# Performance work log

Hardware: AMD Instinct MI355X
Metric: run time of the kernel (lower is better)

Reference implementation:

```python
import jax, jax.numpy as jnp
import numpy as np

E = 1024      # embed_dim
H = 16        # num_heads
HD = E // H   # head_dim = 64


def setup_inputs() -> dict:
    key = jax.random.key(0)
    ks = jax.random.split(key, 8)
    T, B, S = 1024, 4, 1024
    return {
        "query": jax.random.normal(ks[0], (T, B, E), jnp.float32),
        "key": jax.random.normal(ks[1], (S, B, E), jnp.float32),
        "value": jax.random.normal(ks[2], (S, B, E), jnp.float32),
        "attn_mask": jax.random.normal(ks[3], (T, S), jnp.float32),
        "key_padding_mask": jax.random.randint(ks[4], (B, S), 0, 2, jnp.int32),
        "in_proj_weight": jax.random.normal(ks[5], (3 * E, E), jnp.float32) * 0.02,
        "in_proj_bias": jnp.zeros((3 * E,), jnp.float32),
        "out_w": jax.random.normal(ks[6], (E, E), jnp.float32) * 0.02,
        "out_b": jnp.zeros((E,), jnp.float32),
    }


def reference(query, key, value, attn_mask, key_padding_mask,
              in_proj_weight, in_proj_bias, out_w, out_b):
    T, B, _ = query.shape
    S = key.shape[0]
    w_q, w_k, w_v = jnp.split(in_proj_weight, 3, axis=0)   # each [E, E]
    b_q, b_k, b_v = jnp.split(in_proj_bias, 3, axis=0)
    q = query @ w_q.T + b_q                                # [T, B, E]
    k = key @ w_k.T + b_k                                  # [S, B, E]
    v = value @ w_v.T + b_v                                # [S, B, E]
    # [len, B, E] -> [B*H, len, HD]
    q = q.reshape(T, B * H, HD).transpose(1, 0, 2) / jnp.sqrt(jnp.float32(HD))
    k = k.reshape(S, B * H, HD).transpose(1, 0, 2)
    v = v.reshape(S, B * H, HD).transpose(1, 0, 2)
    scores = jnp.einsum('bth,bsh->bts', q, k)              # [B*H, T, S]
    scores = scores + attn_mask[None]                      # float additive mask
    pad = key_padding_mask.astype(bool)                    # [B, S]
    pad = jnp.broadcast_to(pad[:, None, None, :], (B, H, 1, S)).reshape(B * H, 1, S)
    scores = jnp.where(pad, -jnp.inf, scores)
    weights = jax.nn.softmax(scores, axis=-1)              # dropout p=0 -> identity
    out = jnp.einsum('bts,bsh->bth', weights, v)           # [B*H, T, HD]
    out = out.transpose(1, 0, 2).reshape(T, B, E)
    out = out @ out_w.T + out_b
    weights_avg = weights.reshape(B, H, T, S).mean(axis=1) # sum/H == mean
    return out, weights_avg
```

## Files before the change

### kernel.cpp

```cpp
#include <hip/hip_runtime.h>
#include <stdint.h>

typedef short bf16x8 __attribute__((ext_vector_type(8)));
typedef float f32x4  __attribute__((ext_vector_type(4)));

#define LOG2E_F 1.4426950408889634f
#define QSCALE_F 0.1803368801111204f

__device__ __forceinline__ unsigned short f2bf(float f) {
    unsigned int u = __float_as_uint(f);
    return (unsigned short)((u + 0x7FFFu + ((u >> 16) & 1u)) >> 16);
}

__device__ __forceinline__ unsigned short f2bfu(float f) {
    return (unsigned short)((__float_as_uint(f) + 0x8000u) >> 16);
}

__device__ __forceinline__ uint4 pack8(float4 a, float4 b) {
    union { unsigned short us[8]; uint4 v; } p;
    p.us[0] = f2bf(a.x); p.us[1] = f2bf(a.y); p.us[2] = f2bf(a.z); p.us[3] = f2bf(a.w);
    p.us[4] = f2bf(b.x); p.us[5] = f2bf(b.y); p.us[6] = f2bf(b.z); p.us[7] = f2bf(b.w);
    return p.v;
}

__device__ __forceinline__ void gload_lds16(const unsigned short* g, unsigned short* l) {
    __builtin_amdgcn_global_load_lds(
        (const __attribute__((address_space(1))) void*)g,
        (__attribute__((address_space(3))) void*)l, 16, 0, 0);
}

__device__ __forceinline__ int tauinv(int x) {
    const int j4 = x & 7, hh = x & 32, bb = x & 24;
    if (j4 < 4) return hh + ((bb & 15) >> 2) * 8 + (bb >> 4) * 4 + j4;
    const int b2 = bb + 4;
    return hh + ((b2 & 15) >> 2) * 8 + (b2 >> 4) * 4 + (j4 - 4);
}

__global__ __launch_bounds__(256)
void cvt_kernel(const float* __restrict__ q, const float* __restrict__ k,
                const float* __restrict__ v, const float* __restrict__ w,
                const float* __restrict__ ow,
                uint4* __restrict__ Xb, uint4* __restrict__ Wb, uint4* __restrict__ OWb)
{
    const unsigned g = blockIdx.x * 256 + threadIdx.x;
    const float* src;
    uint4* dst;
    if (g < 1572864u) {
        dst = Xb + g;
        if (g < 524288u)        src = q + (size_t)g * 8;
        else if (g < 1048576u)  src = k + (size_t)(g - 524288u) * 8;
        else                    src = v + (size_t)(g - 1048576u) * 8;
    } else if (g < 1966080u) {
        src = w + (size_t)(g - 1572864u) * 8;
        dst = Wb + (g - 1572864u);
    } else {
        src = ow + (size_t)(g - 1966080u) * 8;
        dst = OWb + (g - 1966080u);
    }
    float4 a = *(const float4*)src;
    float4 b = *(const float4*)(src + 4);
    *dst = pack8(a, b);
}

__global__ __launch_bounds__(256)
void mtr_kernel(const float* __restrict__ m, float* __restrict__ mt)
{
    __shared__ float tile[64][65];
    const int bt = (blockIdx.x & 15) << 6;
    const int bs = (blockIdx.x >> 4) << 6;
    const int tx = threadIdx.x & 63;
    const int ty = threadIdx.x >> 6;
#pragma unroll
    for (int i = 0; i < 64; i += 4)
        tile[ty + i][tx] = m[(size_t)(bt + ty + i) * 1024 + bs + tx];
    __syncthreads();
#pragma unroll
    for (int i = 0; i < 64; i += 4) {
        const int s = bs + ty + i;
        mt[(size_t)(s >> 2) * 4096 + (bt + tx) * 4 + (s & 3)] = tile[tx][ty + i];
    }
}

__global__ __launch_bounds__(256)
void qkv_proj_kernel(const unsigned short* __restrict__ Xb, const unsigned short* __restrict__ Wb,
                     const float* __restrict__ bias,
                     unsigned short* __restrict__ Qb, unsigned short* __restrict__ Kb,
                     unsigned short* __restrict__ Vtb)
{
    const int z = blockIdx.z;
    const int j   = blockIdx.x;
    const int xcd = j & 7, idx = j >> 3;
    const int row0 = ((xcd << 2) + (idx >> 3)) * 128;
    const int col0 = (idx & 7) * 128;
    const int wofs = z << 10;

    const unsigned short* A = Xb + (size_t)z * 4194304;
    const unsigned short* B = Wb;

    __shared__ __align__(16) unsigned short As[128 * 32];
    __shared__ __align__(16) unsigned short Bs[128 * 32];

    const int tid  = threadIdx.x;
    const int lane = tid & 63;
    const int wv   = tid >> 6;
    const int wr   = wv >> 1, wc = wv & 1;
    const int c16  = lane & 15;
    const int kof  = (lane >> 4) << 3;

    const f32x4 zero4 = {0.f, 0.f, 0.f, 0.f};
    f32x4 acc[4][4];
#pragma unroll
    for (int m = 0; m < 4; ++m)
#pragma unroll
        for (int n = 0; n < 4; ++n) acc[m][n] = zero4;

    const unsigned short* gA = A + (size_t)(row0 + wv * 16 + (lane >> 2)) * 1024 + ((lane & 3) << 3);
    const unsigned short* gB = B + (size_t)(wofs + col0 + wv * 16 + (lane >> 2)) * 1024 + ((lane & 3) << 3);
    unsigned short* lA = As + tid * 8;
    unsigned short* lB = Bs + tid * 8;

    const int arow = wr * 64 + c16;
    const int brow = wc * 64 + c16;

    for (int k0 = 0; k0 < 1024; k0 += 32) {
        __syncthreads();
        gload_lds16(gA + k0,         lA);
        gload_lds16(gA + k0 + 65536, lA + 2048);
        gload_lds16(gB + k0,         lB);
        gload_lds16(gB + k0 + 65536, lB + 2048);
        __syncthreads();

        bf16x8 af[4], bfr[4];
#pragma unroll
        for (int m = 0; m < 4; ++m)
            af[m] = *(const bf16x8*)&As[(arow + m * 16) * 32 + kof];
#pragma unroll
        for (int n = 0; n < 4; ++n)
            bfr[n] = *(const bf16x8*)&Bs[(brow + n * 16) * 32 + kof];
#pragma unroll
        for (int m = 0; m < 4; ++m)
#pragma unroll
            for (int n = 0; n < 4; ++n)
                acc[m][n] = __builtin_amdgcn_mfma_f32_16x16x32_bf16(af[m], bfr[n], acc[m][n], 0, 0, 0);
    }

    const int ccol = c16;
    const int crow = (lane >> 4) << 2;
#pragma unroll
    for (int n = 0; n < 4; ++n) {
        const int gc   = col0 + wc * 64 + n * 16 + ccol;
        const float bv = bias[wofs + gc];
        const int head = gc >> 6, d = gc & 63;
#pragma unroll
        for (int m = 0; m < 4; ++m) {
            const int tt = (row0 + wr * 64 + m * 16 + crow) >> 2;
            if (z == 2) {
                const int R     = tt >> 7;
                const int tileb = (tt >> 6) & 1;
                const int col   = tauinv(tt & 63);
                const int lc    = tileb * 8 + (col >> 3);
                const int jj    = col & 7;
                const int pc    = lc ^ (d & 7);
                const size_t of = ((size_t)(d) << 7) + (pc << 3) + jj;
#pragma unroll
                for (int r = 0; r < 4; ++r) {
                    const int bh = (r << 4) + head;
                    Vtb[(((size_t)bh * 8 + R) << 13) + of] = f2bf(acc[m][n][r] + bv);
                }
            } else {
#pragma unroll
                for (int r = 0; r < 4; ++r) {
                    const int bh = (r << 4) + head;
                    const float vv = acc[m][n][r] + bv;
                    if (z == 0) Qb[((size_t)bh << 16) + ((size_t)tt << 6) + d] = f2bf(vv * QSCALE_F);
                    else        Kb[((size_t)bh << 16) + ((size_t)tt << 6) + d] = f2bf(vv);
                }
            }
        }
    }
}

__global__ __launch_bounds__(512)
void flash_kernel(const unsigned short* __restrict__ Qb, const unsigned short* __restrict__ Kb,
                  const unsigned short* __restrict__ Vtb, const float* __restrict__ maskT,
                  const int* __restrict__ padmask,
                  float* __restrict__ rl_buf, unsigned short* __restrict__ attn_out)
{
    const int j   = blockIdx.x;
    const int xcd = j & 7, idx = j >> 3;
    const int bh  = xcd * 8 + (idx >> 3);
    const int t0  = (idx & 7) << 7;
    const int b   = bh >> 4, h = bh & 15;

    __shared__ __align__(16) unsigned short Ks[2][2][64 * 64];
    __shared__ __align__(16) unsigned short Vs[2][64 * 128];

    const int tid  = threadIdx.x;
    const int lane = tid & 63;
    const int wv   = tid >> 6;
    const int kof  = (lane >> 4) << 3;
    const int gq   = lane >> 4;
    const int c16  = lane & 15;
    const int g4   = gq << 2;

    const unsigned short* Qbase = Qb  + ((size_t)bh << 16);
    const unsigned short* Kbase = Kb  + ((size_t)bh << 16);
    const unsigned short* Vsig  = Vtb + ((size_t)bh << 16);

    bf16x8 qf[2];
#pragma unroll
    for (int kk = 0; kk < 2; ++kk)
        qf[kk] = *(const bf16x8*)(Qbase + ((size_t)(t0 + wv * 16 + c16) << 6) + kk * 32 + kof);

    const bf16x8 ones = {16256, 16256, 16256, 16256, 16256, 16256, 16256, 16256};

    const f32x4 zero4 = {0.f, 0.f, 0.f, 0.f};
    f32x4 acco[4];
#pragma unroll
    for (int nd = 0; nd < 4; ++nd) acco[nd] = zero4;
    f32x4 acc_l = zero4;

    const int strow = tid >> 3;
    const unsigned short* gK = Kbase + ((size_t)strow << 6) + (((tid & 7) ^ (strow & 7)) << 3);
    unsigned short* lK0a = &Ks[0][0][tid * 8];
    unsigned short* lK0b = &Ks[0][1][tid * 8];
    unsigned short* lK1a = &Ks[1][0][tid * 8];
    unsigned short* lK1b = &Ks[1][1][tid * 8];
    unsigned short* lV0  = &Vs[0][tid * 8];
    unsigned short* lV1  = &Vs[1][tid * 8];

    const int tr2 = t0 + wv * 16 + c16;

    gload_lds16(gK,        lK0a);
    gload_lds16(gK + 4096, lK0b);
    gload_lds16(Vsig + tid * 8,        lV0);
    gload_lds16(Vsig + 4096 + tid * 8, lV0 + 4096);
    __syncthreads();

    for (int rd = 0; rd < 8; ++rd) {
        const int cur = rd & 1;
        const int s0  = rd << 7;

        if (rd < 7) {
            const size_t kofs = (size_t)(s0 + 128) << 6;
            gload_lds16(gK + kofs,        cur ? lK0a : lK1a);
            gload_lds16(gK + kofs + 4096, cur ? lK0b : lK1b);
            const size_t vofs = (size_t)(rd + 1) << 13;
            gload_lds16(Vsig + vofs + tid * 8,        cur ? lV0 : lV1);
            gload_lds16(Vsig + vofs + 4096 + tid * 8, (cur ? lV0 : lV1) + 4096);
        }

        f32x4 accsA[4], accsB[4];
#pragma unroll
        for (int n = 0; n < 4; ++n) { accsA[n] = zero4; accsB[n] = zero4; }
        __builtin_amdgcn_s_setprio(1);
#pragma unroll
        for (int n = 0; n < 4; ++n) {
            const int rowK = n * 16 + c16;
            const int swzK = rowK & 7;
            const int o0 = rowK * 64 + ((gq ^ swzK) << 3);
            const int o1 = rowK * 64 + (((4 + gq) ^ swzK) << 3);
            bf16x8 kfA0 = *(const bf16x8*)&Ks[cur][0][o0];
            bf16x8 kfA1 = *(const bf16x8*)&Ks[cur][0][o1];
            accsA[n] = __builtin_amdgcn_mfma_f32_16x16x32_bf16(kfA0, qf[0], accsA[n], 0, 0, 0);
            accsA[n] = __builtin_amdgcn_mfma_f32_16x16x32_bf16(kfA1, qf[1], accsA[n], 0, 0, 0);
            bf16x8 kfB0 = *(const bf16x8*)&Ks[cur][1][o0];
            bf16x8 kfB1 = *(const bf16x8*)&Ks[cur][1][o1];
            accsB[n] = __builtin_amdgcn_mfma_f32_16x16x32_bf16(kfB0, qf[0], accsB[n], 0, 0, 0);
            accsB[n] = __builtin_amdgcn_mfma_f32_16x16x32_bf16(kfB1, qf[1], accsB[n], 0, 0, 0);
        }
        __builtin_amdgcn_s_setprio(0);

#pragma unroll
        for (int tile = 0; tile < 2; ++tile) {
            const int s0t = s0 + tile * 64;
            f32x4* accs = tile ? accsB : accsA;

            float4 mk[4];
            int4 pd[4];
#pragma unroll
            for (int n = 0; n < 4; ++n) {
                const int srow = s0t + n * 16 + g4;
                pd[n] = *(const int4*)(padmask + (b << 10) + srow);
                mk[n] = *(const float4*)(maskT + (size_t)(srow >> 2) * 4096 + tr2 * 4);
            }

            union { unsigned short us[16]; bf16x8 v[2]; } pk;
#pragma unroll
            for (int n = 0; n < 4; ++n) {
                float x0 = fmaf(mk[n].x, LOG2E_F, accs[n][0]);
                float x1 = fmaf(mk[n].y, LOG2E_F, accs[n][1]);
                float x2 = fmaf(mk[n].z, LOG2E_F, accs[n][2]);
                float x3 = fmaf(mk[n].w, LOG2E_F, accs[n][3]);
                if (pd[n].x) x0 = -1e30f;
                if (pd[n].y) x1 = -1e30f;
                if (pd[n].z) x2 = -1e30f;
                if (pd[n].w) x3 = -1e30f;
                pk.us[n * 4 + 0] = f2bfu(__builtin_amdgcn_exp2f(x0));
                pk.us[n * 4 + 1] = f2bfu(__builtin_amdgcn_exp2f(x1));
                pk.us[n * 4 + 2] = f2bfu(__builtin_amdgcn_exp2f(x2));
                pk.us[n * 4 + 3] = f2bfu(__builtin_amdgcn_exp2f(x3));
            }

            __builtin_amdgcn_s_setprio(1);
#pragma unroll
            for (int hhh = 0; hhh < 2; ++hhh) {
                bf16x8 pf = pk.v[hhh];
                const int lc = tile * 8 + hhh * 4 + gq;
#pragma unroll
                for (int nd = 0; nd < 4; ++nd) {
                    const int rowV = nd * 16 + c16;
                    bf16x8 vf = *(const bf16x8*)&Vs[cur][rowV * 128 + ((lc ^ (rowV & 7)) << 3)];
                    acco[nd] = __builtin_amdgcn_mfma_f32_16x16x32_bf16(pf, vf, acco[nd], 0, 0, 0);
                }
                acc_l = __builtin_amdgcn_mfma_f32_16x16x32_bf16(pf, ones, acc_l, 0, 0, 0);
            }
            __builtin_amdgcn_s_setprio(0);
        }

        if (rd < 7) __syncthreads();
    }

#pragma unroll
    for (int r = 0; r < 4; ++r) {
        const int t = t0 + wv * 16 + g4 + r;
        const float rl = 1.0f / acc_l[r];
        if (c16 == 0)
            rl_buf[(bh << 10) + t] = rl;
#pragma unroll
        for (int nd = 0; nd < 4; ++nd) {
            const int d = nd * 16 + c16;
            attn_out[((size_t)t * 4 + b) * 1024 + h * 64 + d] = f2bf(acco[nd][r] * rl);
        }
    }
}

__global__ __launch_bounds__(256)
void wavg_kernel(const unsigned short* __restrict__ Qb, const unsigned short* __restrict__ Kb,
                 const float* __restrict__ attn_mask, const int* __restrict__ padmask,
                 const float* __restrict__ rl_buf, float* __restrict__ wout)
{
    const int j   = blockIdx.x;
    const int xcd = j & 7;
    const int b   = xcd >> 1;
    const int rr  = ((j >> 3) << 1) + (xcd & 1);
    const int t0  = (rr >> 4) << 6;
    const int s0  = (rr & 15) << 6;

    __shared__ __align__(16) unsigned short Qs[2][64 * 72];
    __shared__ __align__(16) unsigned short Ks2[2][64 * 72];

    const int tid  = threadIdx.x;
    const int lane = tid & 63;
    const int wv   = tid >> 6;
    const int wr   = wv >> 1, wc = wv & 1;
    const int kof  = (lane >> 4) << 3;
    const int srow_st = tid >> 2;
    const int scol_st = (tid & 3) << 4;

    const int t_base = t0 + wr * 32 + ((lane >> 4) << 2);
    const int s_base = s0 + wc * 32 + (lane & 15);

    int pad2[2];
#pragma unroll
    for (int nn = 0; nn < 2; ++nn) pad2[nn] = padmask[(b << 10) + s_base + nn * 16];

    float maskv[2][2][4];
#pragma unroll
    for (int mm = 0; mm < 2; ++mm)
#pragma unroll
        for (int r = 0; r < 4; ++r)
#pragma unroll
            for (int nn = 0; nn < 2; ++nn)
                maskv[mm][nn][r] = attn_mask[(size_t)(t_base + mm * 16 + r) * 1024 + s_base + nn * 16] * LOG2E_F;

    float wsum[2][2][4];
#pragma unroll
    for (int mm = 0; mm < 2; ++mm)
#pragma unroll
        for (int nn = 0; nn < 2; ++nn)
#pragma unroll
            for (int r = 0; r < 4; ++r) wsum[mm][nn][r] = 0.f;

    const unsigned short* qsrc = Qb + ((size_t)(t0 + srow_st) << 6) + scol_st;
    const unsigned short* ksrc = Kb + ((size_t)(s0 + srow_st) << 6) + scol_st;
    const size_t bh0 = (size_t)(b << 4) << 16;

    uint4 q0 = *(const uint4*)(qsrc + bh0);
    uint4 q1 = *(const uint4*)(qsrc + bh0 + 8);
    uint4 k0 = *(const uint4*)(ksrc + bh0);
    uint4 k1 = *(const uint4*)(ksrc + bh0 + 8);
    *(uint4*)&Qs[0][srow_st * 72 + scol_st]      = q0;
    *(uint4*)&Qs[0][srow_st * 72 + scol_st + 8]  = q1;
    *(uint4*)&Ks2[0][srow_st * 72 + scol_st]     = k0;
    *(uint4*)&Ks2[0][srow_st * 72 + scol_st + 8] = k1;
    q0 = *(const uint4*)(qsrc + bh0 + 65536);
    q1 = *(const uint4*)(qsrc + bh0 + 65536 + 8);
    k0 = *(const uint4*)(ksrc + bh0 + 65536);
    k1 = *(const uint4*)(ksrc + bh0 + 65536 + 8);
    __syncthreads();

#pragma unroll 2
    for (int h = 0; h < 16; ++h) {
        const int cur = h & 1;
        const int bh  = (b << 4) + h;

        if (h < 15) {
            *(uint4*)&Qs[cur ^ 1][srow_st * 72 + scol_st]      = q0;
            *(uint4*)&Qs[cur ^ 1][srow_st * 72 + scol_st + 8]  = q1;
            *(uint4*)&Ks2[cur ^ 1][srow_st * 72 + scol_st]     = k0;
            *(uint4*)&Ks2[cur ^ 1][srow_st * 72 + scol_st + 8] = k1;
        }
        if (h < 14) {
            const size_t of = bh0 + (size_t)(h + 2) * 65536;
            q0 = *(const uint4*)(qsrc + of);
            q1 = *(const uint4*)(qsrc + of + 8);
            k0 = *(const uint4*)(ksrc + of);
            k1 = *(const uint4*)(ksrc + of + 8);
        }

        float rlv[2][4];
#pragma unroll
        for (int mm = 0; mm < 2; ++mm)
#pragma unroll
            for (int r = 0; r < 4; ++r)
                rlv[mm][r] = rl_buf[(bh << 10) + t_base + mm * 16 + r];

        const f32x4 zero4 = {0.f, 0.f, 0.f, 0.f};
        f32x4 accs[2][2];
#pragma unroll
        for (int mm = 0; mm < 2; ++mm)
#pragma unroll
            for (int nn = 0; nn < 2; ++nn) accs[mm][nn] = zero4;
#pragma unroll
        for (int nn = 0; nn < 2; ++nn) {
            bf16x8 kf0 = *(const bf16x8*)&Ks2[cur][(wc * 32 + nn * 16 + (lane & 15)) * 72 + kof];
            bf16x8 kf1 = *(const bf16x8*)&Ks2[cur][(wc * 32 + nn * 16 + (lane & 15)) * 72 + 32 + kof];
#pragma unroll
            for (int mm = 0; mm < 2; ++mm) {
                bf16x8 qf0 = *(const bf16x8*)&Qs[cur][(wr * 32 + mm * 16 + (lane & 15)) * 72 + kof];
                bf16x8 qf1 = *(const bf16x8*)&Qs[cur][(wr * 32 + mm * 16 + (lane & 15)) * 72 + 32 + kof];
                accs[mm][nn] = __builtin_amdgcn_mfma_f32_16x16x32_bf16(qf0, kf0, accs[mm][nn], 0, 0, 0);
                accs[mm][nn] = __builtin_amdgcn_mfma_f32_16x16x32_bf16(qf1, kf1, accs[mm][nn], 0, 0, 0);
            }
        }
#pragma unroll
        for (int mm = 0; mm < 2; ++mm)
#pragma unroll
            for (int nn = 0; nn < 2; ++nn)
#pragma unroll
                for (int r = 0; r < 4; ++r)
                    if (!pad2[nn]) {
                        float x = accs[mm][nn][r] + maskv[mm][nn][r];
                        wsum[mm][nn][r] += __builtin_amdgcn_exp2f(x) * rlv[mm][r];
                    }

        if (h < 15) __syncthreads();
    }

#pragma unroll
    for (int mm = 0; mm < 2; ++mm)
#pragma unroll
        for (int nn = 0; nn < 2; ++nn)
#pragma unroll
            for (int r = 0; r < 4; ++r)
                wout[((size_t)b << 20) + (size_t)(t_base + mm * 16 + r) * 1024 + s_base + nn * 16]
                    = wsum[mm][nn][r] * 0.0625f;
}

__global__ __launch_bounds__(256)
void out_proj_kernel(const unsigned short* __restrict__ A, const unsigned short* __restrict__ Wb,
                     const float* __restrict__ bias, float* __restrict__ out)
{
    const int j   = blockIdx.x;
    const int xcd = j & 7, idx = j >> 3;
    const int row0 = ((xcd << 2) + (idx >> 3)) * 128;
    const int col0 = (idx & 7) * 128;

    __shared__ __align__(16) unsigned short As[128 * 32];
    __shared__ __align__(16) unsigned short Bs[128 * 32];

    const int tid  = threadIdx.x;
    const int lane = tid & 63;
    const int wv   = tid >> 6;
    const int wr   = wv >> 1, wc = wv & 1;
    const int c16  = lane & 15;
    const int kof  = (lane >> 4) << 3;

    const f32x4 zero4 = {0.f, 0.f, 0.f, 0.f};
    f32x4 acc[4][4];
#pragma unroll
    for (int m = 0; m < 4; ++m)
#pragma unroll
        for (int n = 0; n < 4; ++n) acc[m][n] = zero4;

    const unsigned short* gA = A  + (size_t)(row0 + wv * 16 + (lane >> 2)) * 1024 + ((lane & 3) << 3);
    const unsigned short* gB = Wb + (size_t)(col0 + wv * 16 + (lane >> 2)) * 1024 + ((lane & 3) << 3);
    unsigned short* lA = As + tid * 8;
    unsigned short* lB = Bs + tid * 8;

    const int arow = wr * 64 + c16;
    const int brow = wc * 64 + c16;

    for (int k0 = 0; k0 < 1024; k0 += 32) {
        __syncthreads();
        gload_lds16(gA + k0,         lA);
        gload_lds16(gA + k0 + 65536, lA + 2048);
        gload_lds16(gB + k0,         lB);
        gload_lds16(gB + k0 + 65536, lB + 2048);
        __syncthreads();

        bf16x8 af[4], bfr[4];
#pragma unroll
        for (int m = 0; m < 4; ++m)
            af[m] = *(const bf16x8*)&As[(arow + m * 16) * 32 + kof];
#pragma unroll
        for (int n = 0; n < 4; ++n)
            bfr[n] = *(const bf16x8*)&Bs[(brow + n * 16) * 32 + kof];
#pragma unroll
        for (int m = 0; m < 4; ++m)
#pragma unroll
            for (int n = 0; n < 4; ++n)
                acc[m][n] = __builtin_amdgcn_mfma_f32_16x16x32_bf16(af[m], bfr[n], acc[m][n], 0, 0, 0);
    }

    const int ccol = c16;
    const int crow = (lane >> 4) << 2;
#pragma unroll
    for (int n = 0; n < 4; ++n) {
        const int gc   = col0 + wc * 64 + n * 16 + ccol;
        const float bv = bias[gc];
#pragma unroll
        for (int m = 0; m < 4; ++m) {
#pragma unroll
            for (int r = 0; r < 4; ++r) {
                const int gr = row0 + wr * 64 + m * 16 + crow + r;
                out[(size_t)gr * 1024 + gc] = acc[m][n][r] + bv;
            }
        }
    }
}

extern "C" void kernel_launch(void* const* d_in, const int* in_sizes, int n_in,
                              void* d_out, int out_size, void* d_ws, size_t ws_size,
                              hipStream_t stream)
{
    const float* query     = (const float*)d_in[0];
    const float* key       = (const float*)d_in[1];
    const float* value     = (const float*)d_in[2];
    const float* attn_mask = (const float*)d_in[3];
    const int*   padmask   = (const int*)  d_in[4];
    const float* in_proj_w = (const float*)d_in[5];
    const float* in_proj_b = (const float*)d_in[6];
    const float* out_w     = (const float*)d_in[7];
    const float* out_b     = (const float*)d_in[8];

    float* out  = (float*)d_out;
    float* wavg = out + 4194304;

    char* ws = (char*)d_ws;
    unsigned short* Qb     = (unsigned short*)(ws);
    unsigned short* Kb     = (unsigned short*)(ws + 8388608);
    unsigned short* Vtb    = (unsigned short*)(ws + 16777216);
    unsigned short* Xb     = (unsigned short*)(ws + 25165824);
    unsigned short* attn_o = (unsigned short*)(ws + 25165824);
    float*          maskT  = (float*)(ws + 33554432);
    unsigned short* Wb     = (unsigned short*)(ws + 50331648);
    unsigned short* OWb    = (unsigned short*)(ws + 56623104);
    float*          rl_buf = (float*)(ws + 58720256);

    cvt_kernel<<<dim3(8192), 256, 0, stream>>>(query, key, value, in_proj_w, out_w,
                                               (uint4*)Xb, (uint4*)Wb, (uint4*)OWb);
    qkv_proj_kernel<<<dim3(256, 1, 3), 256, 0, stream>>>(Xb, Wb, in_proj_b, Qb, Kb, Vtb);
    mtr_kernel<<<dim3(256), 256, 0, stream>>>(attn_mask, maskT);
    flash_kernel<<<dim3(512), 512, 0, stream>>>(Qb, Kb, Vtb, maskT, padmask,
                                                rl_buf, attn_o);
    wavg_kernel<<<dim3(1024), 256, 0, stream>>>(Qb, Kb, attn_mask, padmask,
                                                rl_buf, wavg);
    out_proj_kernel<<<dim3(256), 256, 0, stream>>>(attn_o, OWb, out_b, out);
}
```

Measured before the change: 140.2 us.

## Merge weight-averaging and output projection into one interleaved launch

Combines the wavg kernel and the out_proj GEMM into a single launch of 1280 blocks. Every fifth block runs the output projection and the rest compute averaged attention weights. Both paths share one dynamic shared-memory buffer. The intent is to remove one kernel launch and its tail, and to overlap the memory-bound weight-averaging work with the MFMA-bound projection. In exchange, shared memory per block grows to the larger footprint, which could lower occupancy for the out_proj blocks, and the block-index remapping adds a little integer math.

```diff
diff --git a/kernel.cpp b/kernel.cpp
--- a/kernel.cpp
+++ b/kernel.cpp
@@ -336,208 +336,205 @@
 }
 
 __global__ __launch_bounds__(256)
-void wavg_kernel(const unsigned short* __restrict__ Qb, const unsigned short* __restrict__ Kb,
-                 const float* __restrict__ attn_mask, const int* __restrict__ padmask,
-                 const float* __restrict__ rl_buf, float* __restrict__ wout)
+void wavg_out_kernel(const unsigned short* __restrict__ Qb, const unsigned short* __restrict__ Kb,
+                     const float* __restrict__ attn_mask, const int* __restrict__ padmask,
+                     const float* __restrict__ rl_buf, float* __restrict__ wout,
+                     const unsigned short* __restrict__ A, const unsigned short* __restrict__ OWb,
+                     const float* __restrict__ obias, float* __restrict__ out)
 {
-    const int j   = blockIdx.x;
-    const int xcd = j & 7;
-    const int b   = xcd >> 1;
-    const int rr  = ((j >> 3) << 1) + (xcd & 1);
-    const int t0  = (rr >> 4) << 6;
-    const int s0  = (rr & 15) << 6;
-
-    __shared__ __align__(16) unsigned short Qs[2][64 * 72];
-    __shared__ __align__(16) unsigned short Ks2[2][64 * 72];
-
+    __shared__ __align__(16) unsigned char smem[36864];
+
+    const int jj = blockIdx.x;
     const int tid  = threadIdx.x;
     const int lane = tid & 63;
     const int wv   = tid >> 6;
     const int wr   = wv >> 1, wc = wv & 1;
     const int kof  = (lane >> 4) << 3;
-    const int srow_st = tid >> 2;
-    const int scol_st = (tid & 3) << 4;
-
-    const int t_base = t0 + wr * 32 + ((lane >> 4) << 2);
-    const int s_base = s0 + wc * 32 + (lane & 15);
-
-    int pad2[2];
-#pragma unroll
-    for (int nn = 0; nn < 2; ++nn) pad2[nn] = padmask[(b << 10) + s_base + nn * 16];
-
-    float maskv[2][2][4];
-#pragma unroll
-    for (int mm = 0; mm < 2; ++mm)
-#pragma unroll
-        for (int r = 0; r < 4; ++r)
+    const int c16  = lane & 15;
+    const f32x4 zero4 = {0.f, 0.f, 0.f, 0.f};
+
+    if (jj % 5 == 4) {
+        const int j   = jj / 5;
+        const int xcd = j & 7, idx = j >> 3;
+        const int row0 = ((xcd << 2) + (idx >> 3)) * 128;
+        const int col0 = (idx & 7) * 128;
+
+        unsigned short* As = (unsigned short*)smem;
+        unsigned short* Bs = (unsigned short*)(smem + 8192);
+
+        f32x4 acc[4][4];
+#pragma unroll
+        for (int m = 0; m < 4; ++m)
+#pragma unroll
+            for (int n = 0; n < 4; ++n) acc[m][n] = zero4;
+
+        const unsigned short* gA = A   + (size_t)(row0 + wv * 16 + (lane >> 2)) * 1024 + ((lane & 3) << 3);
+        const unsigned short* gB = OWb + (size_t)(col0 + wv * 16 + (lane >> 2)) * 1024 + ((lane & 3) << 3);
+        unsigned short* lA = As + tid * 8;
+        unsigned short* lB = Bs + tid * 8;
+
+        const int arow = wr * 64 + c16;
+        const int brow = wc * 64 + c16;
+
+        for (int k0 = 0; k0 < 1024; k0 += 32) {
+            __syncthreads();
+            gload_lds16(gA + k0,         lA);
+            gload_lds16(gA + k0 + 65536, lA + 2048);
+            gload_lds16(gB + k0,         lB);
+            gload_lds16(gB + k0 + 65536, lB + 2048);
+            __syncthreads();
+
+            bf16x8 af[4], bfr[4];
+#pragma unroll
+            for (int m = 0; m < 4; ++m)
+                af[m] = *(const bf16x8*)&As[(arow + m * 16) * 32 + kof];
+#pragma unroll
+            for (int n = 0; n < 4; ++n)
+                bfr[n] = *(const bf16x8*)&Bs[(brow + n * 16) * 32 + kof];
+#pragma unroll
+            for (int m = 0; m < 4; ++m)
+#pragma unroll
+                for (int n = 0; n < 4; ++n)
+                    acc[m][n] = __builtin_amdgcn_mfma_f32_16x16x32_bf16(af[m], bfr[n], acc[m][n], 0, 0, 0);
+        }
+
+        const int crow = (lane >> 4) << 2;
+#pragma unroll
+        for (int n = 0; n < 4; ++n) {
+            const int gc   = col0 + wc * 64 + n * 16 + c16;
+            const float bv = obias[gc];
+#pragma unroll
+            for (int m = 0; m < 4; ++m) {
+#pragma unroll
+                for (int r = 0; r < 4; ++r) {
+                    const int gr = row0 + wr * 64 + m * 16 + crow + r;
+                    out[(size_t)gr * 1024 + gc] = acc[m][n][r] + bv;
+                }
+            }
+        }
+    } else {
+        const int j   = (jj / 5) * 4 + (jj % 5);
+        const int xcd = j & 7;
+        const int b   = xcd >> 1;
+        const int rr  = ((j >> 3) << 1) + (xcd & 1);
+        const int t0  = (rr >> 4) << 6;
+        const int s0  = (rr & 15) << 6;
+
+        unsigned short* QsB = (unsigned short*)smem;
+        unsigned short* KsB = (unsigned short*)(smem + 18432);
+
+        const int srow_st = tid >> 2;
+        const int scol_st = (tid & 3) << 4;
+
+        const int t_base = t0 + wr * 32 + ((lane >> 4) << 2);
+        const int s_base = s0 + wc * 32 + c16;
+
+        int pad2[2];
+#pragma unroll
+        for (int nn = 0; nn < 2; ++nn) pad2[nn] = padmask[(b << 10) + s_base + nn * 16];
+
+        float maskv[2][2][4];
+#pragma unroll
+        for (int mm = 0; mm < 2; ++mm)
+#pragma unroll
+            for (int r = 0; r < 4; ++r)
+#pragma unroll
+                for (int nn = 0; nn < 2; ++nn)
+                    maskv[mm][nn][r] = attn_mask[(size_t)(t_base + mm * 16 + r) * 1024 + s_base + nn * 16] * LOG2E_F;
+
+        float wsum[2][2][4];
+#pragma unroll
+        for (int mm = 0; mm < 2; ++mm)
 #pragma unroll
             for (int nn = 0; nn < 2; ++nn)
-                maskv[mm][nn][r] = attn_mask[(size_t)(t_base + mm * 16 + r) * 1024 + s_base + nn * 16] * LOG2E_F;
-
-    float wsum[2][2][4];
-#pragma unroll
-    for (int mm = 0; mm < 2; ++mm)
-#pragma unroll
-        for (int nn = 0; nn < 2; ++nn)
-#pragma unroll
-            for (int r = 0; r < 4; ++r) wsum[mm][nn][r] = 0.f;
-
-    const unsigned short* qsrc = Qb + ((size_t)(t0 + srow_st) << 6) + scol_st;
-    const unsigned short* ksrc = Kb + ((size_t)(s0 + srow_st) << 6) + scol_st;
-    const size_t bh0 = (size_t)(b << 4) << 16;
-
-    uint4 q0 = *(const uint4*)(qsrc + bh0);
-    uint4 q1 = *(const uint4*)(qsrc + bh0 + 8);
-    uint4 k0 = *(const uint4*)(ksrc + bh0);
-    uint4 k1 = *(const uint4*)(ksrc + bh0 + 8);
-    *(uint4*)&Qs[0][srow_st * 72 + scol_st]      = q0;
-    *(uint4*)&Qs[0][srow_st * 72 + scol_st + 8]  = q1;
-    *(uint4*)&Ks2[0][srow_st * 72 + scol_st]     = k0;
-    *(uint4*)&Ks2[0][srow_st * 72 + scol_st + 8] = k1;
-    q0 = *(const uint4*)(qsrc + bh0 + 65536);
-    q1 = *(const uint4*)(qsrc + bh0 + 65536 + 8);
-    k0 = *(const uint4*)(ksrc + bh0 + 65536);
-    k1 = *(const uint4*)(ksrc + bh0 + 65536 + 8);
-    __syncthreads();
+#pragma unroll
+                for (int r = 0; r < 4; ++r) wsum[mm][nn][r] = 0.f;
+
+        const unsigned short* qsrc = Qb + ((size_t)(t0 + srow_st) << 6) + scol_st;
+        const unsigned short* ksrc = Kb + ((size_t)(s0 + srow_st) << 6) + scol_st;
+        const size_t bh0 = (size_t)(b << 4) << 16;
+
+        uint4 q0 = *(const uint4*)(qsrc + bh0);
+        uint4 q1 = *(const uint4*)(qsrc + bh0 + 8);
+        uint4 k0 = *(const uint4*)(ksrc + bh0);
+        uint4 k1 = *(const uint4*)(ksrc + bh0 + 8);
+        *(uint4*)&QsB[srow_st * 72 + scol_st]      = q0;
+        *(uint4*)&QsB[srow_st * 72 + scol_st + 8]  = q1;
+        *(uint4*)&KsB[srow_st * 72 + scol_st]      = k0;
+        *(uint4*)&KsB[srow_st * 72 + scol_st + 8]  = k1;
+        q0 = *(const uint4*)(qsrc + bh0 + 65536);
+        q1 = *(const uint4*)(qsrc + bh0 + 65536 + 8);
+        k0 = *(const uint4*)(ksrc + bh0 + 65536);
+        k1 = *(const uint4*)(ksrc + bh0 + 65536 + 8);
+        __syncthreads();
 
 #pragma unroll 2
-    for (int h = 0; h < 16; ++h) {
-        const int cur = h & 1;
-        const int bh  = (b << 4) + h;
-
-        if (h < 15) {
-            *(uint4*)&Qs[cur ^ 1][srow_st * 72 + scol_st]      = q0;
-            *(uint4*)&Qs[cur ^ 1][srow_st * 72 + scol_st + 8]  = q1;
-            *(uint4*)&Ks2[cur ^ 1][srow_st * 72 + scol_st]     = k0;
-            *(uint4*)&Ks2[cur ^ 1][srow_st * 72 + scol_st + 8] = k1;
-        }
-        if (h < 14) {
-            const size_t of = bh0 + (size_t)(h + 2) * 65536;
-            q0 = *(const uint4*)(qsrc + of);
-            q1 = *(const uint4*)(qsrc + of + 8);
-            k0 = *(const uint4*)(ksrc + of);
-            k1 = *(const uint4*)(ksrc + of + 8);
-        }
-
-        float rlv[2][4];
+        for (int h = 0; h < 16; ++h) {
+            const int cur = h & 1;
+            const int bh  = (b << 4) + h;
+            const int co  = (cur ^ 1) * 4608;
+            const int ci  = cur * 4608;
+
+            if (h < 15) {
+                *(uint4*)&QsB[co + srow_st * 72 + scol_st]     = q0;
+                *(uint4*)&QsB[co + srow_st * 72 + scol_st + 8] = q1;
+                *(uint4*)&KsB[co + srow_st * 72 + scol_st]     = k0;
+                *(uint4*)&KsB[co + srow_st * 72 + scol_st + 8] = k1;
+            }
+            if (h < 14) {
+                const size_t of = bh0 + (size_t)(h + 2) * 65536;
+                q0 = *(const uint4*)(qsrc + of);
+                q1 = *(const uint4*)(qsrc + of + 8);
+                k0 = *(const uint4*)(ksrc + of);
+                k1 = *(const uint4*)(ksrc + of + 8);
+            }
+
+            float rlv[2][4];
+#pragma unroll
+            for (int mm = 0; mm < 2; ++mm)
+#pragma unroll
+                for (int r = 0; r < 4; ++r)
+                    rlv[mm][r] = rl_buf[(bh << 10) + t_base + mm * 16 + r];
+
+            f32x4 accs[2][2];
+#pragma unroll
+            for (int mm = 0; mm < 2; ++mm)
+#pragma unroll
+                for (int nn = 0; nn < 2; ++nn) accs[mm][nn] = zero4;
+#pragma unroll
+            for (int nn = 0; nn < 2; ++nn) {
+                bf16x8 kf0 = *(const bf16x8*)&KsB[ci + (wc * 32 + nn * 16 + c16) * 72 + kof];
+                bf16x8 kf1 = *(const bf16x8*)&KsB[ci + (wc * 32 + nn * 16 + c16) * 72 + 32 + kof];
+#pragma unroll
+                for (int mm = 0; mm < 2; ++mm) {
+                    bf16x8 qf0 = *(const bf16x8*)&QsB[ci + (wr * 32 + mm * 16 + c16) * 72 + kof];
+                    bf16x8 qf1 = *(const bf16x8*)&QsB[ci + (wr * 32 + mm * 16 + c16) * 72 + 32 + kof];
+                    accs[mm][nn] = __builtin_amdgcn_mfma_f32_16x16x32_bf16(qf0, kf0, accs[mm][nn], 0, 0, 0);
+                    accs[mm][nn] = __builtin_amdgcn_mfma_f32_16x16x32_bf16(qf1, kf1, accs[mm][nn], 0, 0, 0);
+                }
+            }
+#pragma unroll
+            for (int mm = 0; mm < 2; ++mm)
+#pragma unroll
+                for (int nn = 0; nn < 2; ++nn)
+#pragma unroll
+                    for (int r = 0; r < 4; ++r)
+                        if (!pad2[nn]) {
+                            float x = accs[mm][nn][r] + maskv[mm][nn][r];
+                            wsum[mm][nn][r] += __builtin_amdgcn_exp2f(x) * rlv[mm][r];
+                        }
+
+            if (h < 15) __syncthreads();
+        }
+
 #pragma unroll
         for (int mm = 0; mm < 2; ++mm)
 #pragma unroll
-            for (int r = 0; r < 4; ++r)
-                rlv[mm][r] = rl_buf[(bh << 10) + t_base + mm * 16 + r];
-
-        const f32x4 zero4 = {0.f, 0.f, 0.f, 0.f};
-        f32x4 accs[2][2];
-#pragma unroll
-        for (int mm = 0; mm < 2; ++mm)
-#pragma unroll
-            for (int nn = 0; nn < 2; ++nn) accs[mm][nn] = zero4;
-#pragma unroll
-        for (int nn = 0; nn < 2; ++nn) {
-            bf16x8 kf0 = *(const bf16x8*)&Ks2[cur][(wc * 32 + nn * 16 + (lane & 15)) * 72 + kof];
-            bf16x8 kf1 = *(const bf16x8*)&Ks2[cur][(wc * 32 + nn * 16 + (lane & 15)) * 72 + 32 + kof];
-#pragma unroll
-            for (int mm = 0; mm < 2; ++mm) {
-                bf16x8 qf0 = *(const bf16x8*)&Qs[cur][(wr * 32 + mm * 16 + (lane & 15)) * 72 + kof];
-                bf16x8 qf1 = *(const bf16x8*)&Qs[cur][(wr * 32 + mm * 16 + (lane & 15)) * 72 + 32 + kof];
-                accs[mm][nn] = __builtin_amdgcn_mfma_f32_16x16x32_bf16(qf0, kf0, accs[mm][nn], 0, 0, 0);
-                accs[mm][nn] = __builtin_amdgcn_mfma_f32_16x16x32_bf16(qf1, kf1, accs[mm][nn], 0, 0, 0);
-            }
-        }
-#pragma unroll
-        for (int mm = 0; mm < 2; ++mm)
-#pragma unroll
             for (int nn = 0; nn < 2; ++nn)
 #pragma unroll
                 for (int r = 0; r < 4; ++r)
-                    if (!pad2[nn]) {
-                        float x = accs[mm][nn][r] + maskv[mm][nn][r];
-                        wsum[mm][nn][r] += __builtin_amdgcn_exp2f(x) * rlv[mm][r];
-                    }
-
-        if (h < 15) __syncthreads();
-    }
-
-#pragma unroll
-    for (int mm = 0; mm < 2; ++mm)
-#pragma unroll
-        for (int nn = 0; nn < 2; ++nn)
-#pragma unroll
-            for (int r = 0; r < 4; ++r)
-                wout[((size_t)b << 20) + (size_t)(t_base + mm * 16 + r) * 1024 + s_base + nn * 16]
-                    = wsum[mm][nn][r] * 0.0625f;
-}
-
-__global__ __launch_bounds__(256)
-void out_proj_kernel(const unsigned short* __restrict__ A, const unsigned short* __restrict__ Wb,
-                     const float* __restrict__ bias, float* __restrict__ out)
-{
-    const int j   = blockIdx.x;
-    const int xcd = j & 7, idx = j >> 3;
-    const int row0 = ((xcd << 2) + (idx >> 3)) * 128;
-    const int col0 = (idx & 7) * 128;
-
-    __shared__ __align__(16) unsigned short As[128 * 32];
-    __shared__ __align__(16) unsigned short Bs[128 * 32];
-
-    const int tid  = threadIdx.x;
-    const int lane = tid & 63;
-    const int wv   = tid >> 6;
-    const int wr   = wv >> 1, wc = wv & 1;
-    const int c16  = lane & 15;
-    const int kof  = (lane >> 4) << 3;
-
-    const f32x4 zero4 = {0.f, 0.f, 0.f, 0.f};
-    f32x4 acc[4][4];
-#pragma unroll
-    for (int m = 0; m < 4; ++m)
-#pragma unroll
-        for (int n = 0; n < 4; ++n) acc[m][n] = zero4;
-
-    const unsigned short* gA = A  + (size_t)(row0 + wv * 16 + (lane >> 2)) * 1024 + ((lane & 3) << 3);
-    const unsigned short* gB = Wb + (size_t)(col0 + wv * 16 + (lane >> 2)) * 1024 + ((lane & 3) << 3);
-    unsigned short* lA = As + tid * 8;
-    unsigned short* lB = Bs + tid * 8;
-
-    const int arow = wr * 64 + c16;
-    const int brow = wc * 64 + c16;
-
-    for (int k0 = 0; k0 < 1024; k0 += 32) {
-        __syncthreads();
-        gload_lds16(gA + k0,         lA);
-        gload_lds16(gA + k0 + 65536, lA + 2048);
-        gload_lds16(gB + k0,         lB);
-        gload_lds16(gB + k0 + 65536, lB + 2048);
-        __syncthreads();
-
-        bf16x8 af[4], bfr[4];
-#pragma unroll
-        for (int m = 0; m < 4; ++m)
-            af[m] = *(const bf16x8*)&As[(arow + m * 16) * 32 + kof];
-#pragma unroll
-        for (int n = 0; n < 4; ++n)
-            bfr[n] = *(const bf16x8*)&Bs[(brow + n * 16) * 32 + kof];
-#pragma unroll
-        for (int m = 0; m < 4; ++m)
-#pragma unroll
-            for (int n = 0; n < 4; ++n)
-                acc[m][n] = __builtin_amdgcn_mfma_f32_16x16x32_bf16(af[m], bfr[n], acc[m][n], 0, 0, 0);
-    }
-
-    const int ccol = c16;
-    const int crow = (lane >> 4) << 2;
-#pragma unroll
-    for (int n = 0; n < 4; ++n) {
-        const int gc   = col0 + wc * 64 + n * 16 + ccol;
-        const float bv = bias[gc];
-#pragma unroll
-        for (int m = 0; m < 4; ++m) {
-#pragma unroll
-            for (int r = 0; r < 4; ++r) {
-                const int gr = row0 + wr * 64 + m * 16 + crow + r;
-                out[(size_t)gr * 1024 + gc] = acc[m][n][r] + bv;
-            }
-        }
+                    wout[((size_t)b << 20) + (size_t)(t_base + mm * 16 + r) * 1024 + s_base + nn * 16]
+                        = wsum[mm][nn][r] * 0.0625f;
     }
 }
 
@@ -575,7 +572,7 @@
     mtr_kernel<<<dim3(256), 256, 0, stream>>>(attn_mask, maskT);
     flash_kernel<<<dim3(512), 512, 0, stream>>>(Qb, Kb, Vtb, maskT, padmask,
                                                 rl_buf, attn_o);
-    wavg_kernel<<<dim3(1024), 256, 0, stream>>>(Qb, Kb, attn_mask, padmask,
-                                                rl_buf, wavg);
-    out_proj_kernel<<<dim3(256), 256, 0, stream>>>(attn_o, OWb, out_b, out);
-}
+    wavg_out_kernel<<<dim3(1280), 256, 0, stream>>>(Qb, Kb, attn_mask, padmask,
+                                                    rl_buf, wavg,
+                                                    attn_o, OWb, out_b, out);
+}
```

Result: no change. 141.5 us (+0.9%).

## Use direct global-to-LDS loads with XOR-swizzled layout in wavg kernel

Applied to the files above, without the earlier changes.

Replaces the register-staged Q/K tile loads in the weights-average kernel with direct global-to-LDS copies (gload_lds16). It swaps the padded 72-stride LDS layout for an unpadded 64-stride layout with an XOR swizzle on 16-byte chunks to avoid bank conflicts. Prefetch depth drops from two heads ahead (registers) to one head ahead (LDS double buffer), and loop unrolling is removed. This frees registers and VALU/LDS-store instructions, but exposes more load latency per iteration.

```diff
diff --git a/kernel.cpp b/kernel.cpp
--- a/kernel.cpp
+++ b/kernel.cpp
@@ -347,19 +347,18 @@
     const int t0  = (rr >> 4) << 6;
     const int s0  = (rr & 15) << 6;
 
-    __shared__ __align__(16) unsigned short Qs[2][64 * 72];
-    __shared__ __align__(16) unsigned short Ks2[2][64 * 72];
+    __shared__ __align__(16) unsigned short Qs[2][64 * 64];
+    __shared__ __align__(16) unsigned short Ks2[2][64 * 64];
 
     const int tid  = threadIdx.x;
     const int lane = tid & 63;
     const int wv   = tid >> 6;
     const int wr   = wv >> 1, wc = wv & 1;
-    const int kof  = (lane >> 4) << 3;
-    const int srow_st = tid >> 2;
-    const int scol_st = (tid & 3) << 4;
-
-    const int t_base = t0 + wr * 32 + ((lane >> 4) << 2);
-    const int s_base = s0 + wc * 32 + (lane & 15);
+    const int gq   = lane >> 4;
+    const int c16  = lane & 15;
+
+    const int t_base = t0 + wr * 32 + (gq << 2);
+    const int s_base = s0 + wc * 32 + c16;
 
     int pad2[2];
 #pragma unroll
@@ -382,41 +381,34 @@
 #pragma unroll
             for (int r = 0; r < 4; ++r) wsum[mm][nn][r] = 0.f;
 
-    const unsigned short* qsrc = Qb + ((size_t)(t0 + srow_st) << 6) + scol_st;
-    const unsigned short* ksrc = Kb + ((size_t)(s0 + srow_st) << 6) + scol_st;
+    const int srow = tid >> 3;
+    const int xch  = (tid & 7) ^ (srow & 7);
+    const unsigned short* qsrc = Qb + ((size_t)(t0 + srow) << 6) + (xch << 3);
+    const unsigned short* ksrc = Kb + ((size_t)(s0 + srow) << 6) + (xch << 3);
     const size_t bh0 = (size_t)(b << 4) << 16;
-
-    uint4 q0 = *(const uint4*)(qsrc + bh0);
-    uint4 q1 = *(const uint4*)(qsrc + bh0 + 8);
-    uint4 k0 = *(const uint4*)(ksrc + bh0);
-    uint4 k1 = *(const uint4*)(ksrc + bh0 + 8);
-    *(uint4*)&Qs[0][srow_st * 72 + scol_st]      = q0;
-    *(uint4*)&Qs[0][srow_st * 72 + scol_st + 8]  = q1;
-    *(uint4*)&Ks2[0][srow_st * 72 + scol_st]     = k0;
-    *(uint4*)&Ks2[0][srow_st * 72 + scol_st + 8] = k1;
-    q0 = *(const uint4*)(qsrc + bh0 + 65536);
-    q1 = *(const uint4*)(qsrc + bh0 + 65536 + 8);
-    k0 = *(const uint4*)(ksrc + bh0 + 65536);
-    k1 = *(const uint4*)(ksrc + bh0 + 65536 + 8);
+    unsigned short* lQ = &Qs[0][tid * 8];
+    unsigned short* lK = &Ks2[0][tid * 8];
+    const int half = 4096;
+
+    gload_lds16(qsrc + bh0,        lQ);
+    gload_lds16(qsrc + bh0 + 2048, lQ + 2048);
+    gload_lds16(ksrc + bh0,        lK);
+    gload_lds16(ksrc + bh0 + 2048, lK + 2048);
     __syncthreads();
 
-#pragma unroll 2
+    const f32x4 zero4 = {0.f, 0.f, 0.f, 0.f};
+
     for (int h = 0; h < 16; ++h) {
         const int cur = h & 1;
         const int bh  = (b << 4) + h;
 
         if (h < 15) {
-            *(uint4*)&Qs[cur ^ 1][srow_st * 72 + scol_st]      = q0;
-            *(uint4*)&Qs[cur ^ 1][srow_st * 72 + scol_st + 8]  = q1;
-            *(uint4*)&Ks2[cur ^ 1][srow_st * 72 + scol_st]     = k0;
-            *(uint4*)&Ks2[cur ^ 1][srow_st * 72 + scol_st + 8] = k1;
-        }
-        if (h < 14) {
-            const size_t of = bh0 + (size_t)(h + 2) * 65536;
-            q0 = *(const uint4*)(qsrc + of);
-            q1 = *(const uint4*)(qsrc + of + 8);
-            k0 = *(const uint4*)(ksrc + of);
-            k1 = *(const uint4*)(ksrc + of + 8);
+            const size_t of = bh0 + (size_t)(h + 1) * 65536;
+            const int dst = (cur ^ 1) * half;
+            gload_lds16(qsrc + of,        &Qs[0][dst + tid * 8]);
+            gload_lds16(qsrc + of + 2048, &Qs[0][dst + tid * 8 + 2048]);
+            gload_lds16(ksrc + of,        &Ks2[0][dst + tid * 8]);
+            gload_lds16(ksrc + of + 2048, &Ks2[0][dst + tid * 8 + 2048]);
         }
 
         float rlv[2][4];
@@ -426,20 +418,25 @@
             for (int r = 0; r < 4; ++r)
                 rlv[mm][r] = rl_buf[(bh << 10) + t_base + mm * 16 + r];
 
-        const f32x4 zero4 = {0.f, 0.f, 0.f, 0.f};
         f32x4 accs[2][2];
 #pragma unroll
         for (int mm = 0; mm < 2; ++mm)
 #pragma unroll
             for (int nn = 0; nn < 2; ++nn) accs[mm][nn] = zero4;
+
+        const int ci = cur * half;
 #pragma unroll
         for (int nn = 0; nn < 2; ++nn) {
-            bf16x8 kf0 = *(const bf16x8*)&Ks2[cur][(wc * 32 + nn * 16 + (lane & 15)) * 72 + kof];
-            bf16x8 kf1 = *(const bf16x8*)&Ks2[cur][(wc * 32 + nn * 16 + (lane & 15)) * 72 + 32 + kof];
+            const int rowK = wc * 32 + nn * 16 + c16;
+            const int swz  = rowK & 7;
+            bf16x8 kf0 = *(const bf16x8*)&Ks2[0][ci + rowK * 64 + ((gq ^ swz) << 3)];
+            bf16x8 kf1 = *(const bf16x8*)&Ks2[0][ci + rowK * 64 + (((4 + gq) ^ swz) << 3)];
 #pragma unroll
             for (int mm = 0; mm < 2; ++mm) {
-                bf16x8 qf0 = *(const bf16x8*)&Qs[cur][(wr * 32 + mm * 16 + (lane & 15)) * 72 + kof];
-                bf16x8 qf1 = *(const bf16x8*)&Qs[cur][(wr * 32 + mm * 16 + (lane & 15)) * 72 + 32 + kof];
+                const int rowQ = wr * 32 + mm * 16 + c16;
+                const int swq  = rowQ & 7;
+                bf16x8 qf0 = *(const bf16x8*)&Qs[0][ci + rowQ * 64 + ((gq ^ swq) << 3)];
+                bf16x8 qf1 = *(const bf16x8*)&Qs[0][ci + rowQ * 64 + (((4 + gq) ^ swq) << 3)];
                 accs[mm][nn] = __builtin_amdgcn_mfma_f32_16x16x32_bf16(qf0, kf0, accs[mm][nn], 0, 0, 0);
                 accs[mm][nn] = __builtin_amdgcn_mfma_f32_16x16x32_bf16(qf1, kf1, accs[mm][nn], 0, 0, 0);
             }
```

Measured after the change: 140.9 us, median of 3. About the same (+0.4%).
